# Performance work log

Measured on AMD Instinct MI355X. Metric: run time of the kernel, lower is better.

## Reference

```python
import jax, jax.numpy as jnp
import numpy as np

B, S, H, HF, V, L, NB, K = 8, 512, 1024, 512, 32000, 4, 8, 2
EPS = 1e-5


def _ln(x, g, b):
    m = jnp.mean(x, -1, keepdims=True)
    v = jnp.mean((x - m) ** 2, -1, keepdims=True)
    return (x - m) * jax.lax.rsqrt(v + EPS) * g + b


def setup_inputs() -> dict:
    key = jax.random.key(0)
    ks = jax.random.split(key, 12)
    n = lambda i, shape, s=0.02: jax.random.normal(ks[i], shape, jnp.float32) * s
    return {
        "input_ids": jax.random.randint(ks[0], (B, S), 0, V),
        "emb": n(1, (V, H)),
        "pos": n(2, (1, 512, H)),
        "torsion_field": jnp.zeros((1, H), jnp.float32),
        "lm_w": n(3, (H, V)),
        "lm_b": jnp.zeros((V,), jnp.float32),
        "sel_w": n(4, (L, H, NB)),
        "sel_b": jnp.zeros((L, NB), jnp.float32),
        "g1": jnp.ones((L, NB, H), jnp.float32),
        "b1": jnp.zeros((L, NB, H), jnp.float32),
        "attn_w": n(5, (L, NB, H, H)),
        "attn_b": jnp.zeros((L, NB, H), jnp.float32),
        "g2": jnp.ones((L, NB, H), jnp.float32),
        "b2": jnp.zeros((L, NB, H), jnp.float32),
        "ff1_w": n(6, (L, NB, H, HF)),
        "ff1_b": jnp.zeros((L, NB, HF), jnp.float32),
        "ff2_w": n(7, (L, NB, HF, H)),
        "ff2_b": jnp.zeros((L, NB, H), jnp.float32),
        "tg": n(8, (L, NB, H), 0.01),
    }


def _forward(input_ids, emb, pos, torsion_field, lm_w, lm_b, sel_w, sel_b,
             g1, b1, attn_w, attn_b, g2, b2, ff1_w, ff1_b, ff2_w, ff2_b, tg):
    # embedding + positional encoding
    h = emb[input_ids] + pos[:, :input_ids.shape[1], :]        # [B,S,H]
    tf = torsion_field[0]                                      # [H] (zeros buffer)
    PRIORITY = 0.5  # fresh block: success_rate*0.6 + excitement*0.4 = 0.5
    for l in range(L):
        # router: sigmoid(Linear(mean-pooled x)), mixed with block priority; topk on batch row 0
        scores = jax.nn.sigmoid(jnp.mean(h, 1) @ sel_w[l] + sel_b[l])   # [B,NB]
        adj0 = scores[0] * 0.7 + PRIORITY * 0.3                         # [NB]
        _, top_idx = jax.lax.top_k(adj0, K)                             # [K]
        params = jax.tree_util.tree_map(
            lambda p: p[l][top_idx],
            (g1, b1, attn_w, attn_b, g2, b2, ff1_w, ff1_b, ff2_w, ff2_b, tg))

        def blk(carry, p):
            pg1, pb1, pwa, pba, pg2, pb2, pw1, pbf1, pw2, pbf2, ptg = p
            x = carry
            ha = _ln(x, pg1, pb1) @ pwa + pba                           # [B,S,H]
            ha = ha * (1.0 + jax.nn.sigmoid(ptg) * tf)[None, None, :]
            hm = x + 0.5 * ha
            h2 = _ln(hm, pg2, pb2)
            h2 = jax.nn.gelu(h2 @ pw1 + pbf1, approximate=False) @ pw2 + pbf2
            return hm + 0.5 * h2, None

        h, _ = jax.lax.scan(blk, h, params)
        h = 1.5 * h  # h*0.5 + h after each layer
    return h @ lm_w + lm_b                                     # [B,S,V]


def reference(input_ids, emb, pos, torsion_field, lm_w, lm_b, sel_w, sel_b,
              g1, b1, attn_w, attn_b, g2, b2, ff1_w, ff1_b, ff2_w, ff2_b, tg):
    return _forward(input_ids, emb, pos, torsion_field, lm_w, lm_b, sel_w, sel_b,
                    g1, b1, attn_w, attn_b, g2, b2, ff1_w, ff1_b, ff2_w, ff2_b, tg)
```

## Files before the change

kernel.cpp:

```cpp
#include <hip/hip_runtime.h>


typedef unsigned short u16;
typedef short bf16x8 __attribute__((ext_vector_type(8)));
typedef float f32x4 __attribute__((ext_vector_type(4)));

struct __align__(8) u16x4_t { u16 x, y, z, w; };

#define MTOT 4096
#define HDIM 1024
#define HFF  512
#define VOC  32000
#define NLAYER 4
#define NBLK 8

#define VMW(n) asm volatile("s_waitcnt vmcnt(" #n ")" ::: "memory")
#define BARR() do { asm volatile("" ::: "memory"); __builtin_amdgcn_s_barrier(); asm volatile("" ::: "memory"); } while (0)

__device__ __forceinline__ u16 f2bf(float f) {
  unsigned u = __float_as_uint(f);
  unsigned r = u + 0x7FFFu + ((u >> 16) & 1u);
  return (u16)(r >> 16);
}

__device__ __forceinline__ float sigmoidf_(float z) {
  return 1.0f / (1.0f + expf(-z));
}

__device__ __forceinline__ void gload16(const void* g, void* l) {
  __builtin_amdgcn_global_load_lds(
      (const __attribute__((address_space(1))) void*)g,
      (__attribute__((address_space(3))) void*)l, 16, 0, 0);
}

__global__ void embed_kernel(const int* __restrict__ ids,
                             const float* __restrict__ emb,
                             const float* __restrict__ pos,
                             float* __restrict__ x) {
  int row = blockIdx.x;
  int t = threadIdx.x;
  int s = row & 511;
  int id = ids[row];
  float4 e = ((const float4*)(emb + (size_t)id * HDIM))[t];
  float4 p = ((const float4*)(pos + (size_t)s * HDIM))[t];
  float4 r;
  r.x = e.x + p.x; r.y = e.y + p.y; r.z = e.z + p.z; r.w = e.w + p.w;
  ((float4*)(x + (size_t)row * HDIM))[t] = r;
}

__global__ void colsum_kernel(const float* __restrict__ x, float* __restrict__ partial) {
  int j = blockIdx.x;
  int t = threadIdx.x;
  float4 s; s.x = 0.f; s.y = 0.f; s.z = 0.f; s.w = 0.f;
  for (int r = 0; r < 8; ++r) {
    float4 a = ((const float4*)(x + (size_t)(j * 8 + r) * HDIM))[t];
    s.x += a.x; s.y += a.y; s.z += a.z; s.w += a.w;
  }
  ((float4*)(partial + (size_t)j * HDIM))[t] = s;
}

__global__ void router_finalize(const float* __restrict__ partial,
                                const float* __restrict__ selw,
                                const float* __restrict__ selb,
                                const float* __restrict__ tg_l,
                                const float* __restrict__ tf,
                                int* __restrict__ idx_out,
                                float* __restrict__ scale_out) {
  int t = threadIdx.x;
  float s = 0.f;
  for (int j = 0; j < 64; ++j) s += partial[(size_t)j * HDIM + t];
  float mean = s * (1.0f / 512.0f);
  __shared__ float sm[HDIM];
  __shared__ float sc[NBLK];
  __shared__ int sidx[2];
  sm[t] = mean;
  __syncthreads();
  int wave = t >> 6, lane = t & 63;
  if (wave < NBLK) {
    float p = 0.f;
    for (int h = lane; h < HDIM; h += 64) p += sm[h] * selw[h * NBLK + wave];
    for (int o = 32; o; o >>= 1) p += __shfl_down(p, o);
    if (lane == 0) sc[wave] = p;
  }
  __syncthreads();
  if (t == 0) {
    float adj[NBLK];
    for (int i = 0; i < NBLK; ++i) {
      float z = sc[i] + selb[i];
      adj[i] = sigmoidf_(z) * 0.7f + 0.15f;
    }
    int i0 = 0;
    for (int i = 1; i < NBLK; ++i) if (adj[i] > adj[i0]) i0 = i;
    int i1 = -1;
    for (int i = 0; i < NBLK; ++i) {
      if (i == i0) continue;
      if (i1 < 0 || adj[i] > adj[i1]) i1 = i;
    }
    idx_out[0] = i0; idx_out[1] = i1;
    sidx[0] = i0; sidx[1] = i1;
  }
  __syncthreads();
  for (int k = 0; k < 2; ++k) {
    int id = sidx[k];
    float z = tg_l[(size_t)id * HDIM + t];
    scale_out[k * HDIM + t] = 1.0f + sigmoidf_(z) * tf[t];
  }
}

__global__ void transpose_all(const float* __restrict__ aw,
                              const float* __restrict__ f1w,
                              const float* __restrict__ f2w,
                              const int* __restrict__ idx, int slot,
                              u16* __restrict__ wA, u16* __restrict__ w1,
                              u16* __restrict__ w2) {
  __shared__ float tile[32][33];
  int b = blockIdx.x;
  int id = idx[slot];
  const float* src; u16* dst; int K, N, n0, k0;
  if (b < 1024) {
    K = 1024; N = 1024; src = aw + (size_t)id * 1024 * 1024;
    n0 = (b & 31) * 32; k0 = (b >> 5) * 32; dst = wA;
  } else if (b < 1536) {
    int c = b - 1024; K = 1024; N = 512; src = f1w + (size_t)id * 1024 * 512;
    n0 = (c & 15) * 32; k0 = (c >> 4) * 32; dst = w1;
  } else {
    int c = b - 1536; K = 512; N = 1024; src = f2w + (size_t)id * 512 * 1024;
    n0 = (c & 31) * 32; k0 = (c >> 5) * 32; dst = w2;
  }
  int tx = threadIdx.x, ty = threadIdx.y;
#pragma unroll
  for (int j = 0; j < 4; ++j) {
    int kr = k0 + ty + j * 8;
    tile[ty + j * 8][tx] = src[(size_t)kr * N + n0 + tx];
  }
  __syncthreads();
#pragma unroll
  for (int j = 0; j < 4; ++j) {
    int nr = n0 + ty + j * 8;
    dst[(size_t)nr * K + k0 + tx] = f2bf(tile[tx][ty + j * 8]);
  }
}

__global__ void transpose_lm(const float* __restrict__ src, u16* __restrict__ dst) {
  __shared__ float tile[32][33];
  int n0 = blockIdx.x * 32, k0 = blockIdx.y * 32;
  int tx = threadIdx.x, ty = threadIdx.y;
#pragma unroll
  for (int j = 0; j < 4; ++j) {
    int kr = k0 + ty + j * 8;
    tile[ty + j * 8][tx] = src[(size_t)kr * VOC + n0 + tx];
  }
  __syncthreads();
#pragma unroll
  for (int j = 0; j < 4; ++j) {
    int nr = n0 + ty + j * 8;
    dst[(size_t)nr * HDIM + k0 + tx] = f2bf(tile[tx][ty + j * 8]);
  }
}

__global__ void ln_kernel(const float* __restrict__ x,
                          const float* __restrict__ g_base,
                          const float* __restrict__ b_base,
                          const int* __restrict__ idx_ptr, int slot,
                          u16* __restrict__ out) {
  int row = blockIdx.x, t = threadIdx.x;
  size_t off = (size_t)idx_ptr[slot] * HDIM;
  const float* g = g_base + off;
  const float* b = b_base + off;
  float4 v = ((const float4*)(x + (size_t)row * HDIM))[t];
  float s = v.x + v.y + v.z + v.w;
  float q = v.x * v.x + v.y * v.y + v.z * v.z + v.w * v.w;
  for (int o = 32; o; o >>= 1) { s += __shfl_down(s, o); q += __shfl_down(q, o); }
  __shared__ float ss[4], sq[4];
  int wave = t >> 6, lane = t & 63;
  if (lane == 0) { ss[wave] = s; sq[wave] = q; }
  __syncthreads();
  if (t == 0) {
    float S = ss[0] + ss[1] + ss[2] + ss[3];
    float Q = sq[0] + sq[1] + sq[2] + sq[3];
    ss[0] = S * (1.0f / 1024.0f);
    sq[0] = Q * (1.0f / 1024.0f);
  }
  __syncthreads();
  float mean = ss[0];
  float var = sq[0] - mean * mean;
  float rs = rsqrtf(var + 1e-5f);
  float4 gv = ((const float4*)g)[t];
  float4 bv = ((const float4*)b)[t];
  u16x4_t o4;
  o4.x = f2bf((v.x - mean) * rs * gv.x + bv.x);
  o4.y = f2bf((v.y - mean) * rs * gv.y + bv.y);
  o4.z = f2bf((v.z - mean) * rs * gv.z + bv.z);
  o4.w = f2bf((v.w - mean) * rs * gv.w + bv.w);
  ((u16x4_t*)(out + (size_t)row * HDIM))[t] = o4;
}

template <int BM, int BN, int EPI>
__global__ __launch_bounds__(256) void gemm_layer(
    const u16* __restrict__ A, const u16* __restrict__ Bt, int N, int K,
    const float* __restrict__ bias_base, const int* __restrict__ idx_ptr,
    int slot, int bias_stride, const float* __restrict__ scale,
    float* __restrict__ xres, u16* __restrict__ outb, float lscale) {
  constexpr int TM = BM / 2, TN = BN / 2;
  constexpr int FM = TM / 16, FN = TN / 16;
  constexpr int NLD = (BM + BN) / 32;
  __shared__ __align__(16) u16 lds[(BM + BN) * 64];

  const int tid = threadIdx.x, wave = tid >> 6, lane = tid & 63;
  const int m0 = blockIdx.y * BM, n0 = blockIdx.x * BN;
  const int wm = wave >> 1, wn = wave & 1;
  const int fr = lane & 15, g = lane >> 4;
  const float* bias =
      bias_base + (idx_ptr ? (size_t)idx_ptr[slot] * bias_stride : 0);

  const u16* gbase[NLD];
  unsigned ldsoff[NLD];
#pragma unroll
  for (int j = 0; j < NLD; ++j) {
    int lo = (tid + j * 256) * 16;
    int q = (lo >> 4) & 7;
    if (lo < BM * 128) {
      int row = lo >> 7;
      gbase[j] = A + (size_t)(m0 + row) * K + (q ^ (row & 7)) * 8;
    } else {
      int bo = lo - BM * 128;
      int row = bo >> 7;
      gbase[j] = Bt + (size_t)(n0 + row) * K + (q ^ (row & 7)) * 8;
    }
    ldsoff[j] = (unsigned)(lo >> 1);
  }

  unsigned offA[FM][2], offB[FN][2];
#pragma unroll
  for (int mi = 0; mi < FM; ++mi)
#pragma unroll
    for (int kk = 0; kk < 2; ++kk)
      offA[mi][kk] = (unsigned)((wm * TM + mi * 16 + fr) * 128 +
                                (((kk * 4 + g) ^ (fr & 7)) << 4));
#pragma unroll
  for (int ni = 0; ni < FN; ++ni)
#pragma unroll
    for (int kk = 0; kk < 2; ++kk)
      offB[ni][kk] = (unsigned)(BM * 128 + (wn * TN + ni * 16 + fr) * 128 +
                                (((kk * 4 + g) ^ (fr & 7)) << 4));

  f32x4 acc[FM][FN];
#pragma unroll
  for (int i = 0; i < FM; ++i)
#pragma unroll
    for (int j = 0; j < FN; ++j) acc[i][j] = (f32x4){0.f, 0.f, 0.f, 0.f};

  for (int kt = 0; kt < K; kt += 64) {
#pragma unroll
    for (int j = 0; j < NLD; ++j) gload16(gbase[j] + kt, lds + ldsoff[j]);
    __syncthreads();
#pragma unroll
    for (int kk = 0; kk < 2; ++kk) {
      bf16x8 af[FM], bf[FN];
#pragma unroll
      for (int mi = 0; mi < FM; ++mi)
        af[mi] = *(const bf16x8*)((const char*)lds + offA[mi][kk]);
#pragma unroll
      for (int ni = 0; ni < FN; ++ni)
        bf[ni] = *(const bf16x8*)((const char*)lds + offB[ni][kk]);
#pragma unroll
      for (int mi = 0; mi < FM; ++mi)
#pragma unroll
        for (int ni = 0; ni < FN; ++ni)
          acc[mi][ni] = __builtin_amdgcn_mfma_f32_16x16x32_bf16(
              af[mi], bf[ni], acc[mi][ni], 0, 0, 0);
    }
    __syncthreads();
  }

  const int rb = g * 4, cn = fr;
#pragma unroll
  for (int ni = 0; ni < FN; ++ni) {
    int n = n0 + wn * TN + ni * 16 + cn;
    float bv = bias[n];
    float sv = 0.f;
    if (EPI == 0) sv = scale[n];
#pragma unroll
    for (int mi = 0; mi < FM; ++mi) {
#pragma unroll
      for (int r = 0; r < 4; ++r) {
        int m = m0 + wm * TM + mi * 16 + rb + r;
        float c = acc[mi][ni][r] + bv;
        size_t o = (size_t)m * N + n;
        if (EPI == 0) {
          xres[o] = xres[o] + 0.5f * (c * sv);
        } else if (EPI == 1) {
          float ge = 0.5f * c * (1.0f + erff(c * 0.70710678118654752f));
          outb[o] = f2bf(ge);
        } else if (EPI == 2) {
          xres[o] = (xres[o] + 0.5f * c) * lscale;
        } else {
          float v = (xres[o] + 0.5f * c) * lscale;
          xres[o] = v;
          outb[o] = f2bf(v);
        }
      }
    }
  }
}

__global__ __launch_bounds__(512, 2) void gemm_lm(
    const u16* __restrict__ A, const u16* __restrict__ Bt,
    const float* __restrict__ bias, float* __restrict__ out) {
  constexpr int K = HDIM;
  constexpr int N = VOC;
  constexpr int NT = K / 32;
  __shared__ __align__(16) u16 smbuf[4 * 16384];

  const int tid = threadIdx.x, wid = tid >> 6, lane = tid & 63;
  const int bid = blockIdx.x;
  const int vbid = (bid & 7) * 250 + (bid >> 3);
  const int n0 = (vbid >> 4) * 256;
  const int m0 = (vbid & 15) * 256;
  const int wm = wid >> 2, wn = wid & 3;
  const int fr = lane & 15, g = lane >> 4;

  const int gsw = ((tid & 3) ^ ((tid >> 3) & 3)) * 8;
  const int srow = tid >> 2;
  const u16* gsrc[4];
  gsrc[0] = A + (size_t)(m0 + srow) * K + gsw;
  gsrc[1] = A + (size_t)(m0 + srow + 128) * K + gsw;
  gsrc[2] = Bt + (size_t)(n0 + srow) * K + gsw;
  gsrc[3] = Bt + (size_t)(n0 + srow + 128) * K + gsw;

  const int swzf = (fr >> 1) & 3;
  unsigned offA[8], offB[4];
#pragma unroll
  for (int mi = 0; mi < 8; ++mi)
    offA[mi] = (unsigned)((wm * 128 + mi * 16 + fr) * 64 + ((g ^ swzf) << 4));
#pragma unroll
  for (int ni = 0; ni < 4; ++ni)
    offB[ni] = (unsigned)(16384 + (wn * 64 + ni * 16 + fr) * 64 +
                          ((g ^ swzf) << 4));

  f32x4 acc[8][4];
#pragma unroll
  for (int i = 0; i < 8; ++i)
#pragma unroll
    for (int j = 0; j < 4; ++j) acc[i][j] = (f32x4){0.f, 0.f, 0.f, 0.f};

#pragma unroll
  for (int s = 0; s < 3; ++s) {
    u16* dst = smbuf + s * 16384 + wid * 512;
    gload16(gsrc[0] + s * 32, dst);
    gload16(gsrc[1] + s * 32, dst + 4096);
    gload16(gsrc[2] + s * 32, dst + 8192);
    gload16(gsrc[3] + s * 32, dst + 12288);
  }

  for (int t = 0; t < NT; ++t) {
    if (t < NT - 2) { VMW(8); } else if (t == NT - 2) { VMW(4); } else { VMW(0); }
    BARR();
    if (t + 3 < NT) {
      u16* dst = smbuf + ((t + 3) & 3) * 16384 + wid * 512;
      const int ko = (t + 3) * 32;
      gload16(gsrc[0] + ko, dst);
      gload16(gsrc[1] + ko, dst + 4096);
      gload16(gsrc[2] + ko, dst + 8192);
      gload16(gsrc[3] + ko, dst + 12288);
    }
    const char* cb = (const char*)smbuf + (size_t)(t & 3) * 32768;
    bf16x8 bv[4], av[8];
#pragma unroll
    for (int ni = 0; ni < 4; ++ni) bv[ni] = *(const bf16x8*)(cb + offB[ni]);
#pragma unroll
    for (int mi = 0; mi < 8; ++mi) av[mi] = *(const bf16x8*)(cb + offA[mi]);
    __builtin_amdgcn_s_setprio(1);
#pragma unroll
    for (int mi = 0; mi < 8; ++mi)
#pragma unroll
      for (int ni = 0; ni < 4; ++ni)
        acc[mi][ni] = __builtin_amdgcn_mfma_f32_16x16x32_bf16(
            av[mi], bv[ni], acc[mi][ni], 0, 0, 0);
    __builtin_amdgcn_s_setprio(0);
  }

  const int rb = g * 4, cn = fr;
#pragma unroll
  for (int ni = 0; ni < 4; ++ni) {
    int n = n0 + wn * 64 + ni * 16 + cn;
    float bvv = bias[n];
#pragma unroll
    for (int mi = 0; mi < 8; ++mi) {
#pragma unroll
      for (int r = 0; r < 4; ++r) {
        int m = m0 + wm * 128 + mi * 16 + rb + r;
        __builtin_nontemporal_store(acc[mi][ni][r] + bvv,
                                    &out[(size_t)m * N + n]);
      }
    }
  }
}

extern "C" void kernel_launch(void* const* d_in, const int* in_sizes, int n_in,
                              void* d_out, int out_size, void* d_ws,
                              size_t ws_size, hipStream_t stream) {
  (void)in_sizes; (void)n_in; (void)out_size; (void)ws_size;
  const int*   ids    = (const int*)d_in[0];
  const float* emb    = (const float*)d_in[1];
  const float* pos    = (const float*)d_in[2];
  const float* tf     = (const float*)d_in[3];
  const float* lm_w   = (const float*)d_in[4];
  const float* lm_b   = (const float*)d_in[5];
  const float* sel_w  = (const float*)d_in[6];
  const float* sel_b  = (const float*)d_in[7];
  const float* g1     = (const float*)d_in[8];
  const float* b1     = (const float*)d_in[9];
  const float* attn_w = (const float*)d_in[10];
  const float* attn_b = (const float*)d_in[11];
  const float* g2     = (const float*)d_in[12];
  const float* b2     = (const float*)d_in[13];
  const float* ff1_w  = (const float*)d_in[14];
  const float* ff1_b  = (const float*)d_in[15];
  const float* ff2_w  = (const float*)d_in[16];
  const float* ff2_b  = (const float*)d_in[17];
  const float* tg     = (const float*)d_in[18];
  float* out = (float*)d_out;

  char* ws = (char*)d_ws;
  float* x       = (float*)(ws + 0);
  u16*   abf     = (u16*)(ws + 16777216);
  u16*   tbuf    = (u16*)(ws + 25165824);
  u16*   wA      = (u16*)(ws + 29360128);
  u16*   w1      = (u16*)(ws + 31457280);
  u16*   w2      = (u16*)(ws + 32505856);
  u16*   lmT     = (u16*)(ws + 33554432);
  float* partial = (float*)(ws + 99090432);
  float* scalev  = (float*)(ws + 99352576);
  int*   idx     = (int*)(ws + 99360768);

  embed_kernel<<<MTOT, 256, 0, stream>>>(ids, emb, pos, x);
  transpose_lm<<<dim3(1000, 32), dim3(32, 8), 0, stream>>>(lm_w, lmT);

  for (int l = 0; l < NLAYER; ++l) {
    colsum_kernel<<<64, 256, 0, stream>>>(x, partial);
    router_finalize<<<1, 1024, 0, stream>>>(
        partial, sel_w + (size_t)l * HDIM * NBLK, sel_b + l * NBLK,
        tg + (size_t)l * NBLK * HDIM, tf, idx, scalev);
    const float* aw_l  = attn_w + (size_t)l * NBLK * HDIM * HDIM;
    const float* f1w_l = ff1_w + (size_t)l * NBLK * HDIM * HFF;
    const float* f2w_l = ff2_w + (size_t)l * NBLK * HFF * HDIM;
    for (int k = 0; k < 2; ++k) {
      transpose_all<<<2048, dim3(32, 8), 0, stream>>>(aw_l, f1w_l, f2w_l, idx,
                                                      k, wA, w1, w2);
      ln_kernel<<<MTOT, 256, 0, stream>>>(x, g1 + (size_t)l * NBLK * HDIM,
                                          b1 + (size_t)l * NBLK * HDIM, idx, k,
                                          abf);
      gemm_layer<128, 64, 0><<<dim3(16, 32), 256, 0, stream>>>(
          abf, wA, HDIM, HDIM, attn_b + (size_t)l * NBLK * HDIM, idx, k, HDIM,
          scalev + k * HDIM, x, nullptr, 1.0f);
      ln_kernel<<<MTOT, 256, 0, stream>>>(x, g2 + (size_t)l * NBLK * HDIM,
                                          b2 + (size_t)l * NBLK * HDIM, idx, k,
                                          abf);
      gemm_layer<64, 64, 1><<<dim3(8, 64), 256, 0, stream>>>(
          abf, w1, HFF, HDIM, ff1_b + (size_t)l * NBLK * HFF, idx, k, HFF,
          nullptr, nullptr, tbuf, 1.0f);
      float lsc = (k == 1) ? 1.5f : 1.0f;
      if (l == NLAYER - 1 && k == 1) {
        gemm_layer<128, 64, 3><<<dim3(16, 32), 256, 0, stream>>>(
            tbuf, w2, HDIM, HFF, ff2_b + (size_t)l * NBLK * HDIM, idx, k, HDIM,
            nullptr, x, abf, lsc);
      } else {
        gemm_layer<128, 64, 2><<<dim3(16, 32), 256, 0, stream>>>(
            tbuf, w2, HDIM, HFF, ff2_b + (size_t)l * NBLK * HDIM, idx, k, HDIM,
            nullptr, x, nullptr, lsc);
      }
    }
  }

  gemm_lm<<<2000, 512, 0, stream>>>(abf, lmT, lm_b, out);
}
```

Baseline: 1.044 ms.

## Restructure LM-head GEMM into double-buffered BK=64 with interleaved sub-tile loads

The vocab projection GEMM now steps through K in 64-wide tiles with two LDS buffers instead of 32-wide tiles with four. Next-tile global loads are split into four chunks, each issued between the four MFMA sub-phases of the current tile, and the LDS swizzle is changed to an 8-way XOR. The aim is to halve the loop iterations and barriers and overlap memory with compute more evenly, at the cost of a second barrier per iteration and more complex vmcnt accounting.

```diff
diff --git a/kernel.cpp b/kernel.cpp
--- a/kernel.cpp
+++ b/kernel.cpp
@@ -309,8 +309,8 @@
     const float* __restrict__ bias, float* __restrict__ out) {
   constexpr int K = HDIM;
   constexpr int N = VOC;
-  constexpr int NT = K / 32;
-  __shared__ __align__(16) u16 smbuf[4 * 16384];
+  constexpr int NT = K / 64;
+  __shared__ __align__(16) u16 smbuf[2 * 32768];
 
   const int tid = threadIdx.x, wid = tid >> 6, lane = tid & 63;
   const int bid = blockIdx.x;
@@ -320,23 +320,32 @@
   const int wm = wid >> 2, wn = wid & 3;
   const int fr = lane & 15, g = lane >> 4;
 
-  const int gsw = ((tid & 3) ^ ((tid >> 3) & 3)) * 8;
-  const int srow = tid >> 2;
-  const u16* gsrc[4];
-  gsrc[0] = A + (size_t)(m0 + srow) * K + gsw;
-  gsrc[1] = A + (size_t)(m0 + srow + 128) * K + gsw;
-  gsrc[2] = Bt + (size_t)(n0 + srow) * K + gsw;
-  gsrc[3] = Bt + (size_t)(n0 + srow + 128) * K + gsw;
-
-  const int swzf = (fr >> 1) & 3;
-  unsigned offA[8], offB[4];
+  const int r0 = tid >> 3, q = tid & 7;
+  const int sg = (q ^ (r0 & 7)) * 8;
+  const u16* usrc[4][2];
+  unsigned uoff[4][2];
+  usrc[0][0] = Bt + (size_t)(n0 + r0) * K + sg;        uoff[0][0] = 16384u + tid * 8;
+  usrc[0][1] = Bt + (size_t)(n0 + 64 + r0) * K + sg;   uoff[0][1] = 20480u + tid * 8;
+  usrc[1][0] = Bt + (size_t)(n0 + 128 + r0) * K + sg;  uoff[1][0] = 24576u + tid * 8;
+  usrc[1][1] = Bt + (size_t)(n0 + 192 + r0) * K + sg;  uoff[1][1] = 28672u + tid * 8;
+  usrc[2][0] = A + (size_t)(m0 + r0) * K + sg;         uoff[2][0] = 0u + tid * 8;
+  usrc[2][1] = A + (size_t)(m0 + 128 + r0) * K + sg;   uoff[2][1] = 8192u + tid * 8;
+  usrc[3][0] = A + (size_t)(m0 + 64 + r0) * K + sg;    uoff[3][0] = 4096u + tid * 8;
+  usrc[3][1] = A + (size_t)(m0 + 192 + r0) * K + sg;   uoff[3][1] = 12288u + tid * 8;
+
+  unsigned offA[8][2], offB[4][2];
 #pragma unroll
   for (int mi = 0; mi < 8; ++mi)
-    offA[mi] = (unsigned)((wm * 128 + mi * 16 + fr) * 64 + ((g ^ swzf) << 4));
+#pragma unroll
+    for (int kk = 0; kk < 2; ++kk)
+      offA[mi][kk] = (unsigned)((wm * 128 + mi * 16 + fr) * 128 +
+                                (((kk * 4 + g) ^ (fr & 7)) << 4));
 #pragma unroll
   for (int ni = 0; ni < 4; ++ni)
-    offB[ni] = (unsigned)(16384 + (wn * 64 + ni * 16 + fr) * 64 +
-                          ((g ^ swzf) << 4));
+#pragma unroll
+    for (int kk = 0; kk < 2; ++kk)
+      offB[ni][kk] = (unsigned)(32768 + (wn * 64 + ni * 16 + fr) * 128 +
+                                (((kk * 4 + g) ^ (fr & 7)) << 4));
 
   f32x4 acc[8][4];
 #pragma unroll
@@ -345,38 +354,82 @@
     for (int j = 0; j < 4; ++j) acc[i][j] = (f32x4){0.f, 0.f, 0.f, 0.f};
 
 #pragma unroll
-  for (int s = 0; s < 3; ++s) {
-    u16* dst = smbuf + s * 16384 + wid * 512;
-    gload16(gsrc[0] + s * 32, dst);
-    gload16(gsrc[1] + s * 32, dst + 4096);
-    gload16(gsrc[2] + s * 32, dst + 8192);
-    gload16(gsrc[3] + s * 32, dst + 12288);
+  for (int u = 0; u < 4; ++u) {
+    gload16(usrc[u][0], smbuf + uoff[u][0]);
+    gload16(usrc[u][1], smbuf + uoff[u][1]);
   }
 
   for (int t = 0; t < NT; ++t) {
-    if (t < NT - 2) { VMW(8); } else if (t == NT - 2) { VMW(4); } else { VMW(0); }
+    const char* cb = (const char*)smbuf + (size_t)(t & 1) * 65536;
+    u16* nb = smbuf + ((t + 1) & 1) * 32768;
+    const int ko = (t + 1) * 64;
+    const bool st = (t + 1 < NT);
+    bf16x8 avl[4], avh[4], bv[4];
+    VMW(2);
     BARR();
-    if (t + 3 < NT) {
-      u16* dst = smbuf + ((t + 3) & 3) * 16384 + wid * 512;
-      const int ko = (t + 3) * 32;
-      gload16(gsrc[0] + ko, dst);
-      gload16(gsrc[1] + ko, dst + 4096);
-      gload16(gsrc[2] + ko, dst + 8192);
-      gload16(gsrc[3] + ko, dst + 12288);
-    }
-    const char* cb = (const char*)smbuf + (size_t)(t & 3) * 32768;
-    bf16x8 bv[4], av[8];
-#pragma unroll
-    for (int ni = 0; ni < 4; ++ni) bv[ni] = *(const bf16x8*)(cb + offB[ni]);
-#pragma unroll
-    for (int mi = 0; mi < 8; ++mi) av[mi] = *(const bf16x8*)(cb + offA[mi]);
+#pragma unroll
+    for (int ni = 0; ni < 4; ++ni) bv[ni] = *(const bf16x8*)(cb + offB[ni][0]);
+#pragma unroll
+    for (int mi = 0; mi < 4; ++mi) avl[mi] = *(const bf16x8*)(cb + offA[mi][0]);
+    if (st) {
+      gload16(usrc[0][0] + ko, nb + uoff[0][0]);
+      gload16(usrc[0][1] + ko, nb + uoff[0][1]);
+    }
     __builtin_amdgcn_s_setprio(1);
 #pragma unroll
-    for (int mi = 0; mi < 8; ++mi)
+    for (int mi = 0; mi < 4; ++mi)
 #pragma unroll
       for (int ni = 0; ni < 4; ++ni)
         acc[mi][ni] = __builtin_amdgcn_mfma_f32_16x16x32_bf16(
-            av[mi], bv[ni], acc[mi][ni], 0, 0, 0);
+            avl[mi], bv[ni], acc[mi][ni], 0, 0, 0);
+    __builtin_amdgcn_s_setprio(0);
+    if (t < NT - 1) { VMW(2); } else { VMW(0); }
+    BARR();
+#pragma unroll
+    for (int mi = 0; mi < 4; ++mi)
+      avh[mi] = *(const bf16x8*)(cb + offA[4 + mi][0]);
+    if (st) {
+      gload16(usrc[1][0] + ko, nb + uoff[1][0]);
+      gload16(usrc[1][1] + ko, nb + uoff[1][1]);
+    }
+    __builtin_amdgcn_s_setprio(1);
+#pragma unroll
+    for (int mi = 0; mi < 4; ++mi)
+#pragma unroll
+      for (int ni = 0; ni < 4; ++ni)
+        acc[4 + mi][ni] = __builtin_amdgcn_mfma_f32_16x16x32_bf16(
+            avh[mi], bv[ni], acc[4 + mi][ni], 0, 0, 0);
+    __builtin_amdgcn_s_setprio(0);
+#pragma unroll
+    for (int ni = 0; ni < 4; ++ni) bv[ni] = *(const bf16x8*)(cb + offB[ni][1]);
+#pragma unroll
+    for (int mi = 0; mi < 4; ++mi) avl[mi] = *(const bf16x8*)(cb + offA[mi][1]);
+    if (st) {
+      gload16(usrc[2][0] + ko, nb + uoff[2][0]);
+      gload16(usrc[2][1] + ko, nb + uoff[2][1]);
+    }
+    __builtin_amdgcn_s_setprio(1);
+#pragma unroll
+    for (int mi = 0; mi < 4; ++mi)
+#pragma unroll
+      for (int ni = 0; ni < 4; ++ni)
+        acc[mi][ni] = __builtin_amdgcn_mfma_f32_16x16x32_bf16(
+            avl[mi], bv[ni], acc[mi][ni], 0, 0, 0);
+    __builtin_amdgcn_s_setprio(0);
+#pragma unroll
+    for (int mi = 0; mi < 4; ++mi)
+      avh[mi] = *(const bf16x8*)(cb + offA[4 + mi][1]);
+    if (st) {
+      gload16(usrc[3][0] + ko, nb + uoff[3][0]);
+      gload16(usrc[3][1] + ko, nb + uoff[3][1]);
+    }
+    __builtin_amdgcn_s_setprio(1);
+#pragma unroll
+    for (int mi = 0; mi < 4; ++mi)
+#pragma unroll
+      for (int ni = 0; ni < 4; ++ni)
+        acc[4 + mi][ni] = __builtin_amdgcn_mfma_f32_16x16x32_bf16(
+            avh[mi], bv[ni], acc[4 + mi][ni], 0, 0, 0);
     __builtin_amdgcn_s_setprio(0);
   }
 
```

Result: faster. 1.010 ms (-3.2%).
